# Kernel tuning notes

Measured on AMD Instinct MI355X. Metric: run time of the kernel, lower is better.

## Reference

```python
import jax, jax.numpy as jnp
import numpy as np

H = 2048          # hidden size
NH = 32           # query heads
NKV = 8           # kv heads
HD = H // NH      # head dim = 64
GROUPS = NH // NKV
S = 2048          # seq len
B = 1
SCALE = HD ** -0.5


def _rope_tables(seq, dim, base=10000.0):
    inv = 1.0 / (base ** (np.arange(0, dim, 2, dtype=np.float32) / dim))
    t = np.arange(seq, dtype=np.float32)
    freqs = np.outer(t, inv)                     # [S, dim/2]
    emb = np.concatenate([freqs, freqs], axis=-1)  # [S, dim]
    return jnp.asarray(np.cos(emb)), jnp.asarray(np.sin(emb))


def setup_inputs() -> dict:
    key = jax.random.key(0)
    ks = jax.random.split(key, 5)
    x = jax.random.normal(ks[0], (B, S, H), dtype=jnp.float32)
    wq = jax.random.normal(ks[1], (H, NH * HD), dtype=jnp.float32) * (H ** -0.5)
    wk = jax.random.normal(ks[2], (H, NKV * HD), dtype=jnp.float32) * (H ** -0.5)
    wv = jax.random.normal(ks[3], (H, NKV * HD), dtype=jnp.float32) * (H ** -0.5)
    wo = jax.random.normal(ks[4], (NH * HD, H), dtype=jnp.float32) * (H ** -0.5)
    cos, sin = _rope_tables(S, HD)
    mask = jnp.tril(jnp.ones((S, S), dtype=bool))[None, None]  # causal [1,1,S,S]
    return {"x": x, "wq": wq, "wk": wk, "wv": wv, "wo": wo,
            "cos": cos, "sin": sin, "mask": mask}


def _rotate_half(t):
    t1, t2 = jnp.split(t, 2, axis=-1)
    return jnp.concatenate([-t2, t1], axis=-1)


def reference(x, wq, wk, wv, wo, cos, sin, mask):
    b, s, _ = x.shape
    # projections
    q = (x @ wq).reshape(b, s, NH, HD).transpose(0, 2, 1, 3)    # [B,NH,S,HD]
    k = (x @ wk).reshape(b, s, NKV, HD).transpose(0, 2, 1, 3)   # [B,NKV,S,HD]
    v = (x @ wv).reshape(b, s, NKV, HD).transpose(0, 2, 1, 3)
    # RoPE (cos/sin broadcast over batch and heads)
    c = cos[None, None]; sn = sin[None, None]
    q = q * c + _rotate_half(q) * sn
    k = k * c + _rotate_half(k) * sn
    # GQA: repeat kv heads to match query heads
    k = jnp.repeat(k, GROUPS, axis=1)                           # [B,NH,S,HD]
    v = jnp.repeat(v, GROUPS, axis=1)
    # scores + causal mask + softmax (dropout p=0 -> identity in eval)
    scores = SCALE * jnp.einsum('bhqd,bhkd->bhqk', q, k)
    scores = jnp.where(mask, scores, -jnp.inf)
    attn = jax.nn.softmax(scores, axis=-1)
    out = jnp.einsum('bhqk,bhkd->bhqd', attn, v)
    out = out.transpose(0, 2, 1, 3).reshape(b, s, NH * HD)
    return out @ wo
```

## Files before the change

### kernel.cpp

```cpp
#include <hip/hip_runtime.h>

typedef unsigned short u16;
typedef unsigned u32;
typedef u16 u16x8 __attribute__((ext_vector_type(8)));
typedef u16 u16x4 __attribute__((ext_vector_type(4)));
typedef u32 u32x4 __attribute__((ext_vector_type(4)));
typedef __bf16 bf8 __attribute__((ext_vector_type(8)));
typedef float f32x4 __attribute__((ext_vector_type(4)));
typedef float f32x16 __attribute__((ext_vector_type(16)));

__device__ __forceinline__ u16 f2b(float f) {
  unsigned u = __float_as_uint(f);
  u += 0x7FFFu + ((u >> 16) & 1u);
  return (u16)(u >> 16);
}
__device__ __forceinline__ float b2f(u16 h) {
  return __uint_as_float(((unsigned)h) << 16);
}
__device__ __forceinline__ bf8 asbf8(u16x8 v) {
  return __builtin_bit_cast(bf8, v);
}
__device__ __forceinline__ void gll16(const u16* g, u16* l) {
  __builtin_amdgcn_global_load_lds(
      (const __attribute__((address_space(1))) unsigned*)(g),
      (__attribute__((address_space(3))) unsigned*)(l), 16, 0, 0);
}
__device__ __forceinline__ u32 cvtpk(float lo, float hi) {
  u32 r;
  asm("v_cvt_pk_bf16_f32 %0, %1, %2" : "=v"(r) : "v"(lo), "v"(hi));
  return r;
}
__device__ __forceinline__ void plswap(u32& a, u32& b) {
  asm("v_permlane32_swap_b32 %0, %1" : "+v"(a), "+v"(b));
}
__device__ __forceinline__ float ex2(float x) {
  return __builtin_amdgcn_exp2f(x);
}
#define MFMA32(A,B,C) __builtin_amdgcn_mfma_f32_32x32x16_bf16(A,B,C,0,0,0)


__global__ __launch_bounds__(256) void xconv(const float* __restrict__ x,
                                             u16* __restrict__ xb) {
  int i = (blockIdx.x * 256 + threadIdx.x) * 4;
  float4 v = *(const float4*)(x + i);
  u16x4 o;
  o[0] = f2b(v.x); o[1] = f2b(v.y); o[2] = f2b(v.z); o[3] = f2b(v.w);
  *(u16x4*)(xb + i) = o;
}

__global__ __launch_bounds__(256) void wtrans(const float* __restrict__ in,
                                              u16* __restrict__ out,
                                              int N, int K) {
  __shared__ float tile[32][33];
  int tx = threadIdx.x & 31, ty = threadIdx.x >> 5;
  int n0 = blockIdx.x * 32, k0 = blockIdx.y * 32;
#pragma unroll
  for (int yy = 0; yy < 32; yy += 8)
    tile[ty + yy][tx] = in[(size_t)(k0 + ty + yy) * N + n0 + tx];
  __syncthreads();
#pragma unroll
  for (int yy = 0; yy < 32; yy += 8)
    out[(size_t)(n0 + ty + yy) * K + k0 + tx] = f2b(tile[tx][ty + yy]);
}

__global__ __launch_bounds__(256) void reduce_qkv(u16* __restrict__ p0,
                                                  const u16* __restrict__ p1,
                                                  const float* __restrict__ cs,
                                                  const float* __restrict__ sn) {
  int idx = blockIdx.x * 256 + threadIdx.x;
  int s = idx / 384, c8 = (idx % 384) * 8;
  size_t base = (size_t)s * 3072 + c8;
  if (c8 < 2560) {
    int hc = c8 & 63;
    if (hc >= 32) return;
    u16x8 a0 = *(const u16x8*)(p0 + base);
    u16x8 a1 = *(const u16x8*)(p1 + base);
    u16x8 b0 = *(const u16x8*)(p0 + base + 32);
    u16x8 b1 = *(const u16x8*)(p1 + base + 32);
    u16x8 oa, ob;
#pragma unroll
    for (int e = 0; e < 8; ++e) {
      float va = b2f(a0[e]) + b2f(a1[e]);
      float vb = b2f(b0[e]) + b2f(b1[e]);
      float c1 = cs[s * 64 + hc + e],      s1 = sn[s * 64 + hc + e];
      float c2 = cs[s * 64 + hc + 32 + e], s2 = sn[s * 64 + hc + 32 + e];
      oa[e] = f2b(va * c1 - vb * s1);
      ob[e] = f2b(vb * c2 + va * s2);
    }
    *(u16x8*)(p0 + base)      = oa;
    *(u16x8*)(p0 + base + 32) = ob;
  } else {
    u16x8 a0 = *(const u16x8*)(p0 + base);
    u16x8 a1 = *(const u16x8*)(p1 + base);
    u16x8 o;
#pragma unroll
    for (int e = 0; e < 8; ++e) o[e] = f2b(b2f(a0[e]) + b2f(a1[e]));
    *(u16x8*)(p0 + base) = o;
  }
}

__global__ __launch_bounds__(256) void reduce_out(const u16* __restrict__ p0,
                                                  const u16* __restrict__ p1,
                                                  float* __restrict__ out) {
  int idx = blockIdx.x * 256 + threadIdx.x;
  size_t base = (size_t)idx * 8;
  u16x8 a0 = *(const u16x8*)(p0 + base);
  u16x8 a1 = *(const u16x8*)(p1 + base);
  float4 lo, hi;
  lo.x = b2f(a0[0]) + b2f(a1[0]); lo.y = b2f(a0[1]) + b2f(a1[1]);
  lo.z = b2f(a0[2]) + b2f(a1[2]); lo.w = b2f(a0[3]) + b2f(a1[3]);
  hi.x = b2f(a0[4]) + b2f(a1[4]); hi.y = b2f(a0[5]) + b2f(a1[5]);
  hi.z = b2f(a0[6]) + b2f(a1[6]); hi.w = b2f(a0[7]) + b2f(a1[7]);
  *(float4*)(out + base)     = lo;
  *(float4*)(out + base + 4) = hi;
}

__global__ __launch_bounds__(256) void kvtrans_f(const u16* __restrict__ qkv,
                                                 u16* __restrict__ Kf,
                                                 u16* __restrict__ Vf) {
  int bid = blockIdx.x;
  if (bid < 512) {
    int tid = bid * 256 + threadIdx.x;
    int s = tid >> 6, cc = tid & 63;
    int kh = cc >> 3, c = cc & 7;
    int j = c >> 1, hi = c & 1;
    int b = s >> 5, la = s & 31;
    u16x8 v = *(const u16x8*)(qkv + (size_t)s * 3072 + 2048 + cc * 8);
    *(u16x8*)(Kf + ((((size_t)(kh * 64 + b) * 4 + j) * 2 + hi) * 32 + la) * 8) = v;
  } else {
    int tid = (bid - 512) * 256 + threadIdx.x;
    int s = tid >> 6, cc = tid & 63;
    int kh = cc >> 3, c = cc & 7;
    int m = c >> 2, laB = (c & 3) * 8;
    int b = s >> 5, s5 = s & 31;
    int jj = s5 >> 4, hi = (s5 >> 3) & 1, e = s5 & 7;
    u16x8 v = *(const u16x8*)(qkv + (size_t)s * 3072 + 2560 + cc * 8);
    u16* dst = Vf + (((size_t)(kh * 64 + b) * 4 + m * 2 + jj) * 64 + hi * 32 + laB) * 8 + e;
#pragma unroll
    for (int i = 0; i < 8; ++i) dst[i * 8] = v[i];
  }
}


__global__ __launch_bounds__(256) void gemm_sk(const u16* __restrict__ A,
                                               const u16* __restrict__ Bt,
                                               u16* __restrict__ C0,
                                               u16* __restrict__ C1,
                                               int N, int Kfull, int KH) {
  __shared__ __align__(16) u16 As[128 * 64];
  __shared__ __align__(16) u16 Bs[128 * 64];
  const int t = threadIdx.x;
  const int lane = t & 63, wid = t >> 6;
  const int wm = (wid >> 1) * 64, wn = (wid & 1) * 64;
  const int la = lane & 15, lg = lane >> 4;
  const int m0 = blockIdx.y * 128, n0 = blockIdx.x * 128;
  const int kbeg = blockIdx.z * KH;
  u16* C = blockIdx.z ? C1 : C0;

  const int srow0 = wid * 32 + (lane >> 3);
  const int scolsw = (((lane & 7) ^ (lane >> 3))) * 8;
  const u16* Ap = A + (size_t)(m0 + srow0) * Kfull + kbeg + scolsw;
  const u16* Bp = Bt + (size_t)(n0 + srow0) * Kfull + kbeg + scolsw;
  u16* Adst = &As[wid * 2048];
  u16* Bdst = &Bs[wid * 2048];
  const size_t rstep8 = (size_t)8 * Kfull;

  f32x4 acc[4][4] = {};

  for (int k0 = 0; k0 < KH; k0 += 64) {
    __syncthreads();
#pragma unroll
    for (int cc = 0; cc < 4; ++cc)
      gll16(Ap + k0 + cc * rstep8, Adst + cc * 512);
#pragma unroll
    for (int cc = 0; cc < 4; ++cc)
      gll16(Bp + k0 + cc * rstep8, Bdst + cc * 512);
    __syncthreads();
#pragma unroll
    for (int kk = 0; kk < 2; ++kk) {
      bf8 af[4], bfr[4];
#pragma unroll
      for (int i = 0; i < 4; ++i) {
        const int row = wm + i * 16 + la;
        const int c8 = (kk * 4 + lg) ^ (row & 7);
        af[i] = asbf8(*(const u16x8*)(&As[row * 64 + c8 * 8]));
      }
#pragma unroll
      for (int j = 0; j < 4; ++j) {
        const int row = wn + j * 16 + la;
        const int c8 = (kk * 4 + lg) ^ (row & 7);
        bfr[j] = asbf8(*(const u16x8*)(&Bs[row * 64 + c8 * 8]));
      }
      __builtin_amdgcn_s_setprio(1);
#pragma unroll
      for (int i = 0; i < 4; ++i)
#pragma unroll
        for (int j = 0; j < 4; ++j)
          acc[i][j] = __builtin_amdgcn_mfma_f32_16x16x32_bf16(af[i], bfr[j],
                                                              acc[i][j], 0, 0, 0);
      __builtin_amdgcn_s_setprio(0);
    }
  }

#pragma unroll
  for (int i = 0; i < 4; ++i)
#pragma unroll
    for (int j = 0; j < 4; ++j)
#pragma unroll
      for (int r = 0; r < 4; ++r) {
        int row = m0 + wm + i * 16 + lg * 4 + r;
        int col = n0 + wn + j * 16 + la;
        C[(size_t)row * N + col] = f2b(acc[i][j][r]);
      }
}


#define STEPL(buf, bb) do {                                          \
    const u16* p_ = &smem[(((h2) << 1) | (buf)) * 4096 + lane8];     \
    bf8 K0 = asbf8(*(const u16x8*)(p_));                             \
    bf8 K1 = asbf8(*(const u16x8*)(p_ + 512));                       \
    bf8 K2 = asbf8(*(const u16x8*)(p_ + 1024));                      \
    bf8 K3 = asbf8(*(const u16x8*)(p_ + 1536));                      \
    bf8 V0 = asbf8(*(const u16x8*)(p_ + 2048));                      \
    bf8 V1 = asbf8(*(const u16x8*)(p_ + 2560));                      \
    bf8 V2 = asbf8(*(const u16x8*)(p_ + 3072));                      \
    bf8 V3 = asbf8(*(const u16x8*)(p_ + 3584));                      \
    f32x16 s = {};                                                   \
    __builtin_amdgcn_s_setprio(1);                                   \
    s = MFMA32(K0, qf0, s);                                          \
    s = MFMA32(K1, qf1, s);                                          \
    s = MFMA32(K2, qf2, s);                                          \
    s = MFMA32(K3, qf3, s);                                          \
    __builtin_amdgcn_s_setprio(0);                                   \
    if ((bb) == kmax) {                                              \
      _Pragma("unroll") for (int r = 0; r < 16; ++r) {               \
        int kvr = (bb) * 32 + (r & 3) + 8 * (r >> 2) + 4 * hi;       \
        if (kvr > q0w + la) s[r] = -1e30f;                           \
      }                                                              \
    }                                                                \
    _Pragma("unroll") for (int r = 0; r < 16; ++r)                   \
      s[r] = ex2(s[r] - 32.0f);                                      \
    float z0 = s[0] + s[1],   z1 = s[2] + s[3];                      \
    float z2 = s[4] + s[5],   z3 = s[6] + s[7];                      \
    float z4 = s[8] + s[9],   z5 = s[10] + s[11];                    \
    float z6 = s[12] + s[13], z7 = s[14] + s[15];                    \
    l_run += ((z0 + z1) + (z2 + z3)) + ((z4 + z5) + (z6 + z7));      \
    u32 c0 = cvtpk(s[0], s[1]),   c1 = cvtpk(s[2], s[3]);            \
    u32 c2 = cvtpk(s[4], s[5]),   c3 = cvtpk(s[6], s[7]);            \
    u32 c4 = cvtpk(s[8], s[9]),   c5 = cvtpk(s[10], s[11]);          \
    u32 c6 = cvtpk(s[12], s[13]), c7 = cvtpk(s[14], s[15]);          \
    plswap(c0, c2); plswap(c1, c3); plswap(c4, c6); plswap(c5, c7);  \
    u32x4 t0; t0[0] = c0; t0[1] = c1; t0[2] = c2; t0[3] = c3;        \
    u32x4 t1; t1[0] = c4; t1[1] = c5; t1[2] = c6; t1[3] = c7;        \
    bf8 pa0 = __builtin_bit_cast(bf8, t0);                           \
    bf8 pa1 = __builtin_bit_cast(bf8, t1);                           \
    __builtin_amdgcn_s_setprio(1);                                   \
    o0 = MFMA32(pa0, V0, o0);                                        \
    o0 = MFMA32(pa1, V1, o0);                                        \
    o1 = MFMA32(pa0, V2, o1);                                        \
    o1 = MFMA32(pa1, V3, o1);                                        \
    __builtin_amdgcn_s_setprio(0);                                   \
  } while (0)

#define STG(bb, buf) do {                                            \
    u16* d_ = &smem[((((h2) << 1) | (buf)) * 4096) + wq * 1024];     \
    const u16* kp_ = Kg + (size_t)(bb) * 2048 + wq * 1024 + lane8;   \
    const u16* vp_ = Vg + (size_t)(bb) * 2048 + wq * 1024 + lane8;   \
    gll16(kp_, d_);                                                  \
    gll16(kp_ + 512, d_ + 512);                                      \
    gll16(vp_, d_ + 2048);                                           \
    gll16(vp_ + 512, d_ + 2560);                                     \
  } while (0)

__global__ __launch_bounds__(256, 4) void attn_fwd(const u16* __restrict__ qkv,
                                                   const u16* __restrict__ Kf,
                                                   const u16* __restrict__ Vf,
                                                   u16* __restrict__ aout) {
  const int head = blockIdx.x;
  const int qt = 31 - (int)blockIdx.y;
  const int Q0 = qt * 64;
  const int Kb = qt * 2;
  const int nb = Kb + 2;
  const int ha = nb >> 1;
  const int kh = head >> 2;
  const int t = threadIdx.x;
  const int w = t >> 6, lane = t & 63;
  const int h2 = w >> 1;
  const int wq = w & 1;
  const int la = lane & 31;
  const int hi = lane >> 5;
  const int lane8 = lane * 8;
  const int q0w = Q0 + 32 * wq;
  const int kmax = Kb + wq;

  __shared__ __align__(16) u16 smem[16384];
  __shared__ float lM[4][32];

  bf8 qf0, qf1, qf2, qf3;
  {
    const u16* qp = qkv + (size_t)(q0w + la) * 3072 + head * 64 + hi * 8;
    const float SC = 0.125f * 1.44269504088896340736f;
#define QLOAD(dst, kk) do {                                          \
      u16x8 v = *(const u16x8*)(qp + (kk) * 16);                     \
      u16x8 sv;                                                      \
      _Pragma("unroll") for (int e = 0; e < 8; ++e)                  \
        sv[e] = f2b(b2f(v[e]) * SC);                                 \
      dst = asbf8(sv);                                               \
    } while (0)
    QLOAD(qf0, 0); QLOAD(qf1, 1); QLOAD(qf2, 2); QLOAD(qf3, 3);
#undef QLOAD
  }

  const u16* Kg = Kf + (size_t)kh * 131072;
  const u16* Vg = Vf + (size_t)kh * 131072;

  f32x16 o0 = {}, o1 = {};
  float l_run = 0.f;

  STG(h2 ? ha : 0, 0);
  __syncthreads();

  for (int i = 0; i < ha; ++i) {
    if (i + 1 < ha) STG(h2 ? (ha + i + 1) : (i + 1), (i + 1) & 1);
    const int bb = h2 ? (ha + i) : i;
    if (bb <= kmax) STEPL(i & 1, bb);
    __syncthreads();
  }

  {
    float lt = l_run + __shfl_xor(l_run, 32);
    if (lane < 32) lM[w][lane] = lt;
#pragma unroll
    for (int r = 0; r < 16; ++r) {
      int crow = (r & 3) + 8 * (r >> 2) + 4 * hi;
      smem[(w * 32 + crow) * 72 + la]      = f2b(o0[r]);
      smem[(w * 32 + crow) * 72 + la + 32] = f2b(o1[r]);
    }
  }
  __syncthreads();

#pragma unroll
  for (int it = 0; it < 2; ++it) {
    const int id = t + it * 256;
    const int q = id >> 3, d0 = (id & 7) * 8;
    const int wA = q >> 5, crow = q & 31;
    float inv = 1.0f / (lM[wA][crow] + lM[wA + 2][crow]);
    u16x8 a = *(const u16x8*)&smem[((wA)     * 32 + crow) * 72 + d0];
    u16x8 b = *(const u16x8*)&smem[((wA + 2) * 32 + crow) * 72 + d0];
    u16x8 outv;
#pragma unroll
    for (int j = 0; j < 8; ++j)
      outv[j] = f2b((b2f(a[j]) + b2f(b[j])) * inv);
    *(u16x8*)(aout + (size_t)(Q0 + q) * 2048 + head * 64 + d0) = outv;
  }
}


extern "C" void kernel_launch(void* const* d_in, const int* in_sizes, int n_in,
                              void* d_out, int out_size, void* d_ws, size_t ws_size,
                              hipStream_t stream) {
  (void)in_sizes; (void)n_in; (void)out_size; (void)ws_size;
  const float* x  = (const float*)d_in[0];
  const float* wq = (const float*)d_in[1];
  const float* wk = (const float*)d_in[2];
  const float* wv = (const float*)d_in[3];
  const float* wo = (const float*)d_in[4];
  const float* cs = (const float*)d_in[5];
  const float* sn = (const float*)d_in[6];

  u16* ws    = (u16*)d_ws;
  u16* xb    = ws;
  u16* wqkvT = ws + 4194304;
  u16* qkv   = ws + 10485760;
  u16* woT   = ws + 16777216;
  u16* ext   = ws + 20971520;
  u16* Kf    = wqkvT;
  u16* Vf    = wqkvT + 1048576;
  u16* aout  = xb;
  u16* op0   = qkv;
  u16* op1   = ext;

  xconv<<<4096, 256, 0, stream>>>(x, xb);
  wtrans<<<dim3(64, 64), 256, 0, stream>>>(wq, wqkvT, 2048, 2048);
  wtrans<<<dim3(16, 64), 256, 0, stream>>>(wk, wqkvT + (size_t)2048 * 2048, 512, 2048);
  wtrans<<<dim3(16, 64), 256, 0, stream>>>(wv, wqkvT + (size_t)2560 * 2048, 512, 2048);
  wtrans<<<dim3(64, 64), 256, 0, stream>>>(wo, woT, 2048, 2048);

  gemm_sk<<<dim3(24, 16, 2), 256, 0, stream>>>(xb, wqkvT, qkv, ext, 3072, 2048, 1024);
  reduce_qkv<<<3072, 256, 0, stream>>>(qkv, ext, cs, sn);
  kvtrans_f<<<1024, 256, 0, stream>>>(qkv, Kf, Vf);
  attn_fwd<<<dim3(32, 32), 256, 0, stream>>>(qkv, Kf, Vf, aout);
  gemm_sk<<<dim3(16, 16, 2), 256, 0, stream>>>(aout, woT, op0, op1, 2048, 2048, 1024);
  reduce_out<<<2048, 256, 0, stream>>>(op0, op1, (float*)d_out);
}
```

Before: 140.5 us.

## Fuse prep kernels, fold K/V retiling into reduce, relax attention barriers

The x conversion and four weight transposes are merged into one prep launch. The K/V tile layout write is folded into the split-K reduce/RoPE kernel, which removes the separate kvtrans pass and its extra read of qkv. The attention loop replaces __syncthreads with explicit vmcnt waits plus raw s_barrier, so the next tile's prefetch can stay in flight while the current tile computes. The hand-tuned vmcnt(4) count depends on how many loads STG issues, and a wrong count would risk a data race.

```diff
diff --git a/kernel.cpp b/kernel.cpp
--- a/kernel.cpp
+++ b/kernel.cpp
@@ -39,21 +39,32 @@
 #define MFMA32(A,B,C) __builtin_amdgcn_mfma_f32_32x32x16_bf16(A,B,C,0,0,0)
 
 
-__global__ __launch_bounds__(256) void xconv(const float* __restrict__ x,
-                                             u16* __restrict__ xb) {
-  int i = (blockIdx.x * 256 + threadIdx.x) * 4;
-  float4 v = *(const float4*)(x + i);
-  u16x4 o;
-  o[0] = f2b(v.x); o[1] = f2b(v.y); o[2] = f2b(v.z); o[3] = f2b(v.w);
-  *(u16x4*)(xb + i) = o;
-}
-
-__global__ __launch_bounds__(256) void wtrans(const float* __restrict__ in,
-                                              u16* __restrict__ out,
-                                              int N, int K) {
+__global__ __launch_bounds__(256) void prep_all(const float* __restrict__ x,
+                                                const float* __restrict__ wqp,
+                                                const float* __restrict__ wkp,
+                                                const float* __restrict__ wvp,
+                                                const float* __restrict__ wop,
+                                                u16* __restrict__ xb,
+                                                u16* __restrict__ wqkvT,
+                                                u16* __restrict__ woT) {
+  const int bid = blockIdx.x;
+  if (bid < 4096) {
+    int i = (bid * 256 + threadIdx.x) * 4;
+    float4 v = *(const float4*)(x + i);
+    u16x4 o;
+    o[0] = f2b(v.x); o[1] = f2b(v.y); o[2] = f2b(v.z); o[3] = f2b(v.w);
+    *(u16x4*)(xb + i) = o;
+    return;
+  }
   __shared__ float tile[32][33];
+  const float* in; u16* out; int N, bx, by;
+  if (bid < 8192)       { int b = bid - 4096;  in = wqp; out = wqkvT;                         N = 2048; bx = b & 63; by = b >> 6; }
+  else if (bid < 9216)  { int b = bid - 8192;  in = wkp; out = wqkvT + (size_t)2048 * 2048;   N = 512;  bx = b & 15; by = b >> 4; }
+  else if (bid < 10240) { int b = bid - 9216;  in = wvp; out = wqkvT + (size_t)2560 * 2048;   N = 512;  bx = b & 15; by = b >> 4; }
+  else                  { int b = bid - 10240; in = wop; out = woT;                           N = 2048; bx = b & 63; by = b >> 6; }
+  const int K = 2048;
   int tx = threadIdx.x & 31, ty = threadIdx.x >> 5;
-  int n0 = blockIdx.x * 32, k0 = blockIdx.y * 32;
+  int n0 = bx * 32, k0 = by * 32;
 #pragma unroll
   for (int yy = 0; yy < 32; yy += 8)
     tile[ty + yy][tx] = in[(size_t)(k0 + ty + yy) * N + n0 + tx];
@@ -65,6 +76,8 @@
 
 __global__ __launch_bounds__(256) void reduce_qkv(u16* __restrict__ p0,
                                                   const u16* __restrict__ p1,
+                                                  u16* __restrict__ Kf,
+                                                  u16* __restrict__ Vf,
                                                   const float* __restrict__ cs,
                                                   const float* __restrict__ sn) {
   int idx = blockIdx.x * 256 + threadIdx.x;
@@ -87,15 +100,31 @@
       oa[e] = f2b(va * c1 - vb * s1);
       ob[e] = f2b(vb * c2 + va * s2);
     }
-    *(u16x8*)(p0 + base)      = oa;
-    *(u16x8*)(p0 + base + 32) = ob;
+    if (c8 < 2048) {
+      *(u16x8*)(p0 + base)      = oa;
+      *(u16x8*)(p0 + base + 32) = ob;
+    } else {
+      int kh = (c8 - 2048) >> 6;
+      int d0 = hc;
+      int b = s >> 5, la = s & 31;
+      int j0 = d0 >> 4, hi0 = (d0 >> 3) & 1;
+      size_t f0 = ((((size_t)(kh * 64 + b) * 4 + j0) * 2 + hi0) * 32 + la) * 8;
+      size_t f1 = ((((size_t)(kh * 64 + b) * 4 + j0 + 2) * 2 + hi0) * 32 + la) * 8;
+      *(u16x8*)(Kf + f0) = oa;
+      *(u16x8*)(Kf + f1) = ob;
+    }
   } else {
     u16x8 a0 = *(const u16x8*)(p0 + base);
     u16x8 a1 = *(const u16x8*)(p1 + base);
-    u16x8 o;
-#pragma unroll
-    for (int e = 0; e < 8; ++e) o[e] = f2b(b2f(a0[e]) + b2f(a1[e]));
-    *(u16x8*)(p0 + base) = o;
+    int c = c8 - 2560;
+    int kh = c >> 6, d0 = c & 63;
+    int m = d0 >> 5, la0 = d0 & 31;
+    int b = s >> 5, s5 = s & 31;
+    int jj = s5 >> 4, hi = (s5 >> 3) & 1, e = s5 & 7;
+    u16* dst = Vf + (((size_t)(kh * 64 + b) * 4 + m * 2 + jj) * 64 + hi * 32 + la0) * 8 + e;
+#pragma unroll
+    for (int i = 0; i < 8; ++i)
+      dst[i * 8] = f2b(b2f(a0[i]) + b2f(a1[i]));
   }
 }
 
@@ -113,32 +142,6 @@
   hi.z = b2f(a0[6]) + b2f(a1[6]); hi.w = b2f(a0[7]) + b2f(a1[7]);
   *(float4*)(out + base)     = lo;
   *(float4*)(out + base + 4) = hi;
-}
-
-__global__ __launch_bounds__(256) void kvtrans_f(const u16* __restrict__ qkv,
-                                                 u16* __restrict__ Kf,
-                                                 u16* __restrict__ Vf) {
-  int bid = blockIdx.x;
-  if (bid < 512) {
-    int tid = bid * 256 + threadIdx.x;
-    int s = tid >> 6, cc = tid & 63;
-    int kh = cc >> 3, c = cc & 7;
-    int j = c >> 1, hi = c & 1;
-    int b = s >> 5, la = s & 31;
-    u16x8 v = *(const u16x8*)(qkv + (size_t)s * 3072 + 2048 + cc * 8);
-    *(u16x8*)(Kf + ((((size_t)(kh * 64 + b) * 4 + j) * 2 + hi) * 32 + la) * 8) = v;
-  } else {
-    int tid = (bid - 512) * 256 + threadIdx.x;
-    int s = tid >> 6, cc = tid & 63;
-    int kh = cc >> 3, c = cc & 7;
-    int m = c >> 2, laB = (c & 3) * 8;
-    int b = s >> 5, s5 = s & 31;
-    int jj = s5 >> 4, hi = (s5 >> 3) & 1, e = s5 & 7;
-    u16x8 v = *(const u16x8*)(qkv + (size_t)s * 3072 + 2560 + cc * 8);
-    u16* dst = Vf + (((size_t)(kh * 64 + b) * 4 + m * 2 + jj) * 64 + hi * 32 + laB) * 8 + e;
-#pragma unroll
-    for (int i = 0; i < 8; ++i) dst[i * 8] = v[i];
-  }
 }
 
 
@@ -318,13 +321,18 @@
   float l_run = 0.f;
 
   STG(h2 ? ha : 0, 0);
-  __syncthreads();
 
   for (int i = 0; i < ha; ++i) {
-    if (i + 1 < ha) STG(h2 ? (ha + i + 1) : (i + 1), (i + 1) & 1);
+    const bool pf = (i + 1 < ha);
+    if (pf) STG(h2 ? (ha + i + 1) : (i + 1), (i + 1) & 1);
+    if (pf) asm volatile("s_waitcnt vmcnt(4)" ::: "memory");
+    else    asm volatile("s_waitcnt vmcnt(0)" ::: "memory");
+    __builtin_amdgcn_s_barrier();
+    __builtin_amdgcn_sched_barrier(0);
     const int bb = h2 ? (ha + i) : i;
     if (bb <= kmax) STEPL(i & 1, bb);
-    __syncthreads();
+    __builtin_amdgcn_sched_barrier(0);
+    __builtin_amdgcn_s_barrier();
   }
 
   {
@@ -380,15 +388,10 @@
   u16* op0   = qkv;
   u16* op1   = ext;
 
-  xconv<<<4096, 256, 0, stream>>>(x, xb);
-  wtrans<<<dim3(64, 64), 256, 0, stream>>>(wq, wqkvT, 2048, 2048);
-  wtrans<<<dim3(16, 64), 256, 0, stream>>>(wk, wqkvT + (size_t)2048 * 2048, 512, 2048);
-  wtrans<<<dim3(16, 64), 256, 0, stream>>>(wv, wqkvT + (size_t)2560 * 2048, 512, 2048);
-  wtrans<<<dim3(64, 64), 256, 0, stream>>>(wo, woT, 2048, 2048);
+  prep_all<<<14336, 256, 0, stream>>>(x, wq, wk, wv, wo, xb, wqkvT, woT);
 
   gemm_sk<<<dim3(24, 16, 2), 256, 0, stream>>>(xb, wqkvT, qkv, ext, 3072, 2048, 1024);
-  reduce_qkv<<<3072, 256, 0, stream>>>(qkv, ext, cs, sn);
-  kvtrans_f<<<1024, 256, 0, stream>>>(qkv, Kf, Vf);
+  reduce_qkv<<<3072, 256, 0, stream>>>(qkv, ext, Kf, Vf, cs, sn);
   attn_fwd<<<dim3(32, 32), 256, 0, stream>>>(qkv, Kf, Vf, aout);
   gemm_sk<<<dim3(16, 16, 2), 256, 0, stream>>>(aout, woT, op0, op1, 2048, 2048, 1024);
   reduce_out<<<2048, 256, 0, stream>>>(op0, op1, (float*)d_out);
```

Result: faster. 130.4 us (-7.2%).
